# Kernel tuning notes

Hardware: AMD Instinct MI355X
Metric: run time of the kernel (lower is better)

The kernel has to match this reference:

```python
import jax, jax.numpy as jnp
import numpy as np

N_HEADS = 16
ROPE_BASE = 10000.0


def setup_inputs() -> dict:
    key = jax.random.key(0)
    k1, k2, k3 = jax.random.split(key, 3)
    B, L, D = 2, 2048, 2048
    x = jax.random.normal(k1, (B, L, D), dtype=jnp.float32)
    w_qkv = jax.random.normal(k2, (D, 3 * D), dtype=jnp.float32) * (1.0 / np.sqrt(D))
    w_out = jax.random.normal(k3, (D, D), dtype=jnp.float32) * (1.0 / np.sqrt(D))
    return {"x": x, "w_qkv": w_qkv, "w_out": w_out}


def _rope_cos_sin(L, head_dim, dtype):
    # inv_freq over even dims, freqs duplicated across both halves (HF convention)
    inv_freq = 1.0 / (ROPE_BASE ** (jnp.arange(0, head_dim, 2, dtype=jnp.float32) / head_dim))
    freqs = jnp.arange(L, dtype=jnp.float32)[:, None] * inv_freq[None, :]  # [L, hd/2]
    emb = jnp.concatenate([freqs, freqs], axis=-1)  # [L, hd]
    return jnp.cos(emb).astype(dtype), jnp.sin(emb).astype(dtype)


def _rotate_half(t):
    h = t.shape[-1] // 2
    return jnp.concatenate([-t[..., h:], t[..., :h]], axis=-1)


def reference(x, w_qkv, w_out):
    B, L, D = x.shape
    H = N_HEADS
    hd = D // H
    qkv = x @ w_qkv  # [B, L, 3D]
    q, k, v = jnp.split(qkv, 3, axis=-1)

    def heads(t):  # [B, L, D] -> [B, H, L, hd]
        return t.reshape(B, L, H, hd).transpose(0, 2, 1, 3)

    q, k, v = heads(q), heads(k), heads(v)
    cos, sin = _rope_cos_sin(L, hd, x.dtype)  # [L, hd] broadcast over B,H
    q = q * cos + _rotate_half(q) * sin
    k = k * cos + _rotate_half(k) * sin
    # SDPA, no mask, no dropout (eval), not causal
    scale = 1.0 / np.sqrt(hd)
    scores = jnp.einsum('bhld,bhsd->bhls', q, k) * scale
    attn = jax.nn.softmax(scores, axis=-1)
    y = jnp.einsum('bhls,bhsd->bhld', attn, v)  # [B, H, L, hd]
    y = y.transpose(0, 2, 1, 3).reshape(B, L, D)
    return y @ w_out
```

## Files before the change

kernel.cpp:

```cpp
#include <hip/hip_runtime.h>

typedef __attribute__((ext_vector_type(8))) short bf16x8;
typedef __attribute__((ext_vector_type(8))) unsigned short u16x8;
typedef __attribute__((ext_vector_type(4))) float f32x4;
typedef __attribute__((ext_vector_type(16))) float f32x16;
typedef __attribute__((ext_vector_type(4))) unsigned short u16x4;
typedef __attribute__((ext_vector_type(4))) unsigned int u32x4;
typedef unsigned int u32;

#define BB 2
#define LL 2048
#define DD 2048
#define HH 16
#define HDIM 128
#define MM 4096
#define NQKV 6144

__device__ __forceinline__ unsigned short f2bf(float f) {
    unsigned int u = __builtin_bit_cast(unsigned int, f);
    u += 0x7FFFu + ((u >> 16) & 1u);
    return (unsigned short)(u >> 16);
}
__device__ __forceinline__ float bf2f(unsigned short h) {
    unsigned int u = ((unsigned int)h) << 16;
    return __builtin_bit_cast(float, u);
}

__device__ __forceinline__ void gload16(const unsigned short* g, unsigned short* l) {
    __builtin_amdgcn_global_load_lds((const __attribute__((address_space(1))) void*)g,
                                     (__attribute__((address_space(3))) void*)l, 16, 0, 0);
}

__device__ __forceinline__ u32 cvtpk(float lo, float hi) {
    u32 r;
    asm("v_cvt_pk_bf16_f32 %0, %1, %2" : "=v"(r) : "v"(lo), "v"(hi));
    return r;
}
__device__ __forceinline__ void plswap(u32& a, u32& b) {
    asm("v_permlane32_swap_b32 %0, %1" : "+v"(a), "+v"(b));
}

__global__ __launch_bounds__(256) void k_cvt_bf16(const float* __restrict__ in,
                                                  unsigned short* __restrict__ out,
                                                  int n4) {
    int i = blockIdx.x * 256 + threadIdx.x;
    if (i < n4) {
        float4 v = reinterpret_cast<const float4*>(in)[i];
        u16x4 o;
        o[0] = f2bf(v.x); o[1] = f2bf(v.y); o[2] = f2bf(v.z); o[3] = f2bf(v.w);
        reinterpret_cast<u16x4*>(out)[i] = o;
    }
}

__global__ __launch_bounds__(256) void k_cvt_T(const float* __restrict__ in,
                                               unsigned short* __restrict__ out,
                                               int K, int N) {
    __shared__ unsigned short t[64][72];
    int n0 = blockIdx.x * 64, k0 = blockIdx.y * 64;
    int tid = threadIdx.x;
    int tr = tid >> 4, tc = tid & 15;
    #pragma unroll
    for (int i = 0; i < 4; ++i) {
        int k = i * 16 + tr;
        float4 v = *reinterpret_cast<const float4*>(in + (size_t)(k0 + k) * N + n0 + tc * 4);
        t[tc * 4 + 0][k] = f2bf(v.x);
        t[tc * 4 + 1][k] = f2bf(v.y);
        t[tc * 4 + 2][k] = f2bf(v.z);
        t[tc * 4 + 3][k] = f2bf(v.w);
    }
    __syncthreads();
    #pragma unroll
    for (int i = 0; i < 4; ++i) {
        int n = i * 16 + tr;
        u16x4 o = *reinterpret_cast<u16x4*>(&t[n][tc * 4]);
        *reinterpret_cast<u16x4*>(out + (size_t)(n0 + n) * K + k0 + tc * 4) = o;
    }
}

__global__ __launch_bounds__(256) void k_transV(const unsigned short* __restrict__ in,
                                                unsigned short* __restrict__ out) {
    __shared__ unsigned short t[64][68];
    int l0 = blockIdx.x * 64, d0 = blockIdx.y * 64;
    int bh = blockIdx.z;
    const unsigned short* ib = in + (size_t)bh * LL * HDIM;
    unsigned short* ob = out + (size_t)bh * HDIM * LL;
    int tid = threadIdx.x;
    int tr = tid >> 4, tc = tid & 15;
    #pragma unroll
    for (int i = 0; i < 4; ++i) {
        int l = i * 16 + tr;
        u16x4 v = *reinterpret_cast<const u16x4*>(ib + (size_t)(l0 + l) * HDIM + d0 + tc * 4);
        t[tc * 4 + 0][l] = v[0];
        t[tc * 4 + 1][l] = v[1];
        t[tc * 4 + 2][l] = v[2];
        t[tc * 4 + 3][l] = v[3];
    }
    __syncthreads();
    #pragma unroll
    for (int i = 0; i < 4; ++i) {
        int d = i * 16 + tr;
        u16x4 o = *reinterpret_cast<u16x4*>(&t[d][tc * 4]);
        *reinterpret_cast<u16x4*>(ob + (size_t)(d0 + d) * LL + l0 + tc * 4) = o;
    }
}

__global__ __launch_bounds__(256) void k_rope_table(float* __restrict__ ct,
                                                    float* __restrict__ st) {
    int idx = blockIdx.x * 256 + threadIdx.x;
    if (idx >= LL * 64) return;
    int pos = idx >> 6, d = idx & 63;
    float freq = __expf(-(float)d * (9.210340371976184f / 64.0f));
    float ang = (float)pos * freq;
    ct[idx] = cosf(ang);
    st[idx] = sinf(ang);
}

__global__ __launch_bounds__(256) void k_rope_apply(unsigned short* __restrict__ Q,
                                                    unsigned short* __restrict__ K,
                                                    const float* __restrict__ ct,
                                                    const float* __restrict__ st) {
    int idx = blockIdx.x * 256 + threadIdx.x;
    int d = idx & 63;
    int pos = (idx >> 6) & (LL - 1);
    int bh = idx >> 17;
    size_t base = ((size_t)bh * LL + pos) * HDIM;
    float c = ct[pos * 64 + d], s = st[pos * 64 + d];
    float q0 = bf2f(Q[base + d]), q1 = bf2f(Q[base + d + 64]);
    Q[base + d]      = f2bf(q0 * c - q1 * s);
    Q[base + d + 64] = f2bf(q1 * c + q0 * s);
    float k0 = bf2f(K[base + d]), k1 = bf2f(K[base + d + 64]);
    K[base + d]      = f2bf(k0 * c - k1 * s);
    K[base + d + 64] = f2bf(k1 * c + k0 * s);
}

__global__ __launch_bounds__(512, 2) void k_gemm384(const unsigned short* __restrict__ A,
                                                    const unsigned short* __restrict__ Bt,
                                                    unsigned short* __restrict__ outQ,
                                                    unsigned short* __restrict__ outK,
                                                    unsigned short* __restrict__ outV) {
    __shared__ unsigned short sm[3 * 20480];
    const int Kn = DD;
    const int tid = threadIdx.x;
    const int lane = tid & 63, w = tid >> 6;
    const int wm = w >> 2, wn = w & 3;
    const int lrow = lane & 15, lgrp = lane >> 4;
    const int NT = Kn / 32;

    int orig = blockIdx.x;
    int tau = (orig & 7) * 32 + (orig >> 3);
    const int m0 = (tau & 15) * 256, n0 = (tau >> 4) * 384;

    const int srow = lane >> 2, scol = lane & 3;
    const int scolg = ((scol ^ ((srow >> 1) & 3)) * 8);
    const int fcol  = ((lgrp ^ ((lrow >> 1) & 3)) * 8);

    f32x4 acc[8][6] = {};

    auto stageA = [&](int t, int r) {
        unsigned short* dst = sm + (t % 3) * 20480 + (r * 128 + w * 16) * 32;
        gload16(A + (size_t)(m0 + r * 128 + w * 16 + srow) * Kn + t * 32 + scolg, dst);
    };
    auto stageB = [&](int t, int r) {
        unsigned short* dst = sm + (t % 3) * 20480 + 8192 + (r * 128 + w * 16) * 32;
        gload16(Bt + (size_t)(n0 + r * 128 + w * 16 + srow) * Kn + t * 32 + scolg, dst);
    };

    auto body = [&](int t, bool doStage) {
        unsigned short* bufA = sm + (t % 3) * 20480;
        unsigned short* bufB = bufA + 8192;
        bf16x8 af[8], bfr[2];
        #pragma unroll
        for (int f = 0; f < 8; ++f)
            af[f] = *reinterpret_cast<const bf16x8*>(bufA + (wm * 128 + f * 16 + lrow) * 32 + fcol);
        bfr[0] = *reinterpret_cast<const bf16x8*>(bufB + (wn * 96 + 0 * 16 + lrow) * 32 + fcol);
        bfr[1] = *reinterpret_cast<const bf16x8*>(bufB + (wn * 96 + 1 * 16 + lrow) * 32 + fcol);
        if (doStage) { stageA(t + 2, 0); stageA(t + 2, 1); }
        __builtin_amdgcn_s_barrier();
        __builtin_amdgcn_s_setprio(1);
        #pragma unroll
        for (int fm = 0; fm < 8; ++fm)
            #pragma unroll
            for (int j = 0; j < 2; ++j)
                acc[fm][j] = __builtin_amdgcn_mfma_f32_16x16x32_bf16(af[fm], bfr[j], acc[fm][j], 0, 0, 0);
        __builtin_amdgcn_s_setprio(0);
        bfr[0] = *reinterpret_cast<const bf16x8*>(bufB + (wn * 96 + 2 * 16 + lrow) * 32 + fcol);
        bfr[1] = *reinterpret_cast<const bf16x8*>(bufB + (wn * 96 + 3 * 16 + lrow) * 32 + fcol);
        if (doStage) { stageB(t + 2, 0); stageB(t + 2, 1); }
        __builtin_amdgcn_s_barrier();
        __builtin_amdgcn_s_setprio(1);
        #pragma unroll
        for (int fm = 0; fm < 8; ++fm)
            #pragma unroll
            for (int j = 0; j < 2; ++j)
                acc[fm][2 + j] = __builtin_amdgcn_mfma_f32_16x16x32_bf16(af[fm], bfr[j], acc[fm][2 + j], 0, 0, 0);
        __builtin_amdgcn_s_setprio(0);
        bfr[0] = *reinterpret_cast<const bf16x8*>(bufB + (wn * 96 + 4 * 16 + lrow) * 32 + fcol);
        bfr[1] = *reinterpret_cast<const bf16x8*>(bufB + (wn * 96 + 5 * 16 + lrow) * 32 + fcol);
        if (doStage) { stageB(t + 2, 2); }
        __builtin_amdgcn_s_barrier();
        __builtin_amdgcn_s_setprio(1);
        #pragma unroll
        for (int fm = 0; fm < 8; ++fm)
            #pragma unroll
            for (int j = 0; j < 2; ++j)
                acc[fm][4 + j] = __builtin_amdgcn_mfma_f32_16x16x32_bf16(af[fm], bfr[j], acc[fm][4 + j], 0, 0, 0);
        __builtin_amdgcn_s_setprio(0);
    };

    stageA(0, 0); stageA(0, 1); stageB(0, 0); stageB(0, 1); stageB(0, 2);
    stageA(1, 0); stageA(1, 1); stageB(1, 0); stageB(1, 1); stageB(1, 2);
    asm volatile("s_waitcnt vmcnt(5)" ::: "memory");
    __builtin_amdgcn_s_barrier();

    for (int t = 0; t < NT - 2; ++t) {
        body(t, true);
        asm volatile("s_waitcnt vmcnt(5)" ::: "memory");
        __builtin_amdgcn_s_barrier();
    }
    body(NT - 2, false);
    asm volatile("s_waitcnt vmcnt(0)" ::: "memory");
    __builtin_amdgcn_s_barrier();
    body(NT - 1, false);

    #pragma unroll
    for (int fm = 0; fm < 8; ++fm) {
        int mrow = m0 + wm * 128 + fm * 16 + lgrp * 4;
        #pragma unroll
        for (int fn = 0; fn < 6; ++fn) {
            int ncol = n0 + wn * 96 + fn * 16 + lrow;
            int which = ncol >> 11;
            int rr = ncol & (DD - 1);
            int h = rr >> 7, d = rr & (HDIM - 1);
            unsigned short* dst = (which == 0) ? outQ : ((which == 1) ? outK : outV);
            #pragma unroll
            for (int i = 0; i < 4; ++i) {
                int m = mrow + i;
                int b = m >> 11, pos = m & (LL - 1);
                dst[((size_t)(b * HH + h) * LL + pos) * HDIM + d] = f2bf(acc[fm][fn][i]);
            }
        }
    }
}

__global__ __launch_bounds__(512) void k_gemm2x(const unsigned short* __restrict__ A,
                                                const unsigned short* __restrict__ Bt,
                                                float* __restrict__ outC) {
    __shared__ unsigned short sm[4 * 12288];
    const int Kn = DD, Nn = DD;
    const int tid = threadIdx.x;
    const int lane = tid & 63, w = tid >> 6;
    const int wm = w >> 1, wn = w & 1;
    const int lrow = lane & 15, lgrp = lane >> 4;
    const int NT = Kn / 32;

    int orig = blockIdx.x;
    int tau = (orig & 7) * 32 + (orig >> 3);
    const int m0 = (tau & 15) * 256, n0 = (tau >> 4) * 128;

    const int srow = lane >> 2, scol = lane & 3;
    const int scolg = ((scol ^ ((srow >> 1) & 3)) * 8);
    const int fcol  = ((lgrp ^ ((lrow >> 1) & 3)) * 8);

    f32x4 acc[4][4] = {};

    auto stage = [&](int t) {
        const int kb = t * 32;
        unsigned short* buf = sm + (t & 3) * 12288;
        gload16(A  + (size_t)(m0 + w * 16 + srow) * Kn + kb + scolg,        buf + w * 512);
        gload16(A  + (size_t)(m0 + 128 + w * 16 + srow) * Kn + kb + scolg,  buf + 4096 + w * 512);
        gload16(Bt + (size_t)(n0 + w * 16 + srow) * Kn + kb + scolg,        buf + 8192 + w * 512);
    };

    auto tile_body = [&](int t, bool do_stage) {
        unsigned short* buf = sm + (t & 3) * 12288;
        bf16x8 af[4], bfr[4];
        #pragma unroll
        for (int f = 0; f < 4; ++f)
            af[f] = *reinterpret_cast<const bf16x8*>(buf + (wm * 64 + f * 16 + lrow) * 32 + fcol);
        #pragma unroll
        for (int f = 0; f < 4; ++f)
            bfr[f] = *reinterpret_cast<const bf16x8*>(buf + 8192 + (wn * 64 + f * 16 + lrow) * 32 + fcol);
        if (do_stage) stage(t + 3);
        __builtin_amdgcn_s_barrier();
        __builtin_amdgcn_s_setprio(1);
        #pragma unroll
        for (int fm = 0; fm < 4; ++fm)
            #pragma unroll
            for (int fn = 0; fn < 4; ++fn)
                acc[fm][fn] = __builtin_amdgcn_mfma_f32_16x16x32_bf16(af[fm], bfr[fn], acc[fm][fn], 0, 0, 0);
        __builtin_amdgcn_s_setprio(0);
    };

    stage(0); stage(1); stage(2);
    asm volatile("s_waitcnt vmcnt(6)" ::: "memory");
    __builtin_amdgcn_s_barrier();

    for (int t = 0; t < NT - 3; ++t) {
        tile_body(t, true);
        asm volatile("s_waitcnt vmcnt(6)" ::: "memory");
        __builtin_amdgcn_s_barrier();
    }
    tile_body(NT - 3, false);
    asm volatile("s_waitcnt vmcnt(3)" ::: "memory");
    __builtin_amdgcn_s_barrier();
    tile_body(NT - 2, false);
    asm volatile("s_waitcnt vmcnt(0)" ::: "memory");
    __builtin_amdgcn_s_barrier();
    tile_body(NT - 1, false);

    #pragma unroll
    for (int fm = 0; fm < 4; ++fm) {
        int mrow = m0 + wm * 64 + fm * 16 + lgrp * 4;
        #pragma unroll
        for (int fn = 0; fn < 4; ++fn) {
            int ncol = n0 + wn * 64 + fn * 16 + lrow;
            #pragma unroll
            for (int i = 0; i < 4; ++i)
                outC[(size_t)(mrow + i) * (size_t)Nn + ncol] = acc[fm][fn][i];
        }
    }
}

__global__ __launch_bounds__(256, 2) void k_attn(const unsigned short* __restrict__ Q,
                                                 const unsigned short* __restrict__ K,
                                                 const unsigned short* __restrict__ Vt,
                                                 unsigned short* __restrict__ Y) {
    __shared__ unsigned short Kl[2][64][136];
    __shared__ unsigned short VTl[2][128][72];
    int tid = threadIdx.x;
    int lane = tid & 63, w = tid >> 6;
    int l31 = lane & 31, hl = lane >> 5;
    int orig = blockIdx.x;
    int id = (orig & 7) * 64 + (orig >> 3);
    int bh = id >> 4, qt = id & 15;
    int b = bh >> 4, hh = bh & 15;
    const unsigned short* Qb = Q  + (size_t)bh * LL * HDIM;
    const unsigned short* Kb = K  + (size_t)bh * LL * HDIM;
    const unsigned short* Vb = Vt + (size_t)bh * HDIM * LL;
    int q0 = qt * 128 + w * 32;

    bf16x8 qf[8];
    #pragma unroll
    for (int kk = 0; kk < 8; ++kk)
        qf[kk] = *reinterpret_cast<const bf16x8*>(
            Qb + (size_t)(q0 + l31) * HDIM + kk * 16 + hl * 8);

    f32x16 accO[4] = {};
    f32x16 accL = {};
    bf16x8 ones;
    #pragma unroll
    for (int j = 0; j < 8; ++j) ones[j] = (short)0x3F80;
    const float scale = 0.08838834764831845f;

    u16x8 kr[4], vr[4];
    auto sload = [&](int kt) {
        #pragma unroll
        for (int i = 0; i < 4; ++i) {
            int c = i * 256 + tid;
            kr[i] = *reinterpret_cast<const u16x8*>(Kb + (size_t)(kt * 64 + (c >> 4)) * HDIM + (c & 15) * 8);
            vr[i] = *reinterpret_cast<const u16x8*>(Vb + (size_t)(c >> 3) * LL + kt * 64 + (c & 7) * 8);
        }
    };
    auto swrite = [&](int buf) {
        #pragma unroll
        for (int i = 0; i < 4; ++i) {
            int c = i * 256 + tid;
            *reinterpret_cast<u16x8*>(&Kl[buf][c >> 4][(c & 15) * 8]) = kr[i];
            *reinterpret_cast<u16x8*>(&VTl[buf][c >> 3][(c & 7) * 8]) = vr[i];
        }
    };

    sload(0);
    swrite(0);
    __syncthreads();

    for (int kt = 0; kt < LL / 64; ++kt) {
        int cb = kt & 1;
        if (kt + 1 < LL / 64) sload(kt + 1);

        f32x16 s[2] = {};
        __builtin_amdgcn_s_setprio(1);
        #pragma unroll
        for (int kk = 0; kk < 8; ++kk) {
            bf16x8 kf0 = *reinterpret_cast<const bf16x8*>(&Kl[cb][l31][kk * 16 + hl * 8]);
            bf16x8 kf1 = *reinterpret_cast<const bf16x8*>(&Kl[cb][32 + l31][kk * 16 + hl * 8]);
            s[0] = __builtin_amdgcn_mfma_f32_32x32x16_bf16(kf0, qf[kk], s[0], 0, 0, 0);
            s[1] = __builtin_amdgcn_mfma_f32_32x32x16_bf16(kf1, qf[kk], s[1], 0, 0, 0);
        }
        __builtin_amdgcn_s_setprio(0);

        bf16x8 pa[2][2];
        #pragma unroll
        for (int kn = 0; kn < 2; ++kn) {
            float p[16];
            #pragma unroll
            for (int r = 0; r < 16; ++r) p[r] = __expf(s[kn][r] * scale);
            #pragma unroll
            for (int ksub = 0; ksub < 2; ++ksub) {
                const int bse = ksub * 8;
                u32 a0 = cvtpk(p[bse + 0], p[bse + 1]);
                u32 a1 = cvtpk(p[bse + 2], p[bse + 3]);
                u32 b0 = cvtpk(p[bse + 4], p[bse + 5]);
                u32 b1 = cvtpk(p[bse + 6], p[bse + 7]);
                plswap(a0, b0);
                plswap(a1, b1);
                u32x4 fw; fw[0] = a0; fw[1] = a1; fw[2] = b0; fw[3] = b1;
                pa[kn][ksub] = __builtin_bit_cast(bf16x8, fw);
            }
        }

        __builtin_amdgcn_s_setprio(1);
        #pragma unroll
        for (int kn = 0; kn < 2; ++kn)
            #pragma unroll
            for (int ksub = 0; ksub < 2; ++ksub) {
                accL = __builtin_amdgcn_mfma_f32_32x32x16_bf16(pa[kn][ksub], ones, accL, 0, 0, 0);
                #pragma unroll
                for (int dn = 0; dn < 4; ++dn) {
                    bf16x8 vf = *reinterpret_cast<const bf16x8*>(
                        &VTl[cb][dn * 32 + l31][kn * 32 + ksub * 16 + hl * 8]);
                    accO[dn] = __builtin_amdgcn_mfma_f32_32x32x16_bf16(pa[kn][ksub], vf, accO[dn], 0, 0, 0);
                }
            }
        __builtin_amdgcn_s_setprio(0);

        if (kt + 1 < LL / 64) swrite(cb ^ 1);
        __syncthreads();
    }

    #pragma unroll
    for (int r = 0; r < 16; ++r) {
        float inv = 1.0f / accL[r];
        int qrow = (r & 3) + 8 * (r >> 2) + 4 * hl;
        int pos = q0 + qrow;
        #pragma unroll
        for (int dn = 0; dn < 4; ++dn) {
            int d = dn * 32 + l31;
            Y[((size_t)b * LL + pos) * DD + hh * HDIM + d] = f2bf(accO[dn][r] * inv);
        }
    }
}

extern "C" void kernel_launch(void* const* d_in, const int* in_sizes, int n_in,
                              void* d_out, int out_size, void* d_ws, size_t ws_size,
                              hipStream_t stream) {
    const float* x     = (const float*)d_in[0];
    const float* wqkv  = (const float*)d_in[1];
    const float* wout  = (const float*)d_in[2];
    float* out = (float*)d_out;

    char* ws = (char*)d_ws;
    size_t off = 0;
    auto take = [&](size_t bytes) { char* p = ws + off; off += (bytes + 255) & ~(size_t)255; return p; };
    unsigned short* xb    = (unsigned short*)take((size_t)MM * DD * 2);
    unsigned short* wqkvT = (unsigned short*)take((size_t)DD * NQKV * 2);
    unsigned short* woutT = (unsigned short*)take((size_t)DD * DD * 2);
    unsigned short* Qb    = (unsigned short*)take((size_t)BB * HH * LL * HDIM * 2);
    unsigned short* Kb    = (unsigned short*)take((size_t)BB * HH * LL * HDIM * 2);
    unsigned short* Vb    = (unsigned short*)take((size_t)BB * HH * LL * HDIM * 2);
    unsigned short* Yb    = (unsigned short*)take((size_t)MM * DD * 2);
    float* ct             = (float*)take((size_t)LL * 64 * 4);
    float* st             = (float*)take((size_t)LL * 64 * 4);
    if (off > ws_size) return;
    unsigned short* VtB = xb;

    k_cvt_bf16<<<(MM * DD / 4 + 255) / 256, 256, 0, stream>>>(x, xb, MM * DD / 4);
    k_cvt_T<<<dim3(NQKV / 64, DD / 64), 256, 0, stream>>>(wqkv, wqkvT, DD, NQKV);
    k_cvt_T<<<dim3(DD / 64, DD / 64), 256, 0, stream>>>(wout, woutT, DD, DD);
    k_rope_table<<<(LL * 64 + 255) / 256, 256, 0, stream>>>(ct, st);

    k_gemm384<<<256, 512, 0, stream>>>(xb, wqkvT, Qb, Kb, Vb);
    k_transV<<<dim3(LL / 64, HDIM / 64, BB * HH), 256, 0, stream>>>(Vb, VtB);
    k_rope_apply<<<(BB * HH * LL * 64) / 256, 256, 0, stream>>>(Qb, Kb, ct, st);
    k_attn<<<BB * HH * (LL / 128), 256, 0, stream>>>(Qb, Kb, VtB, Yb);
    k_gemm2x<<<256, 512, 0, stream>>>(Yb, woutT, out);
}
```

Measured before the change: 254.2 us.

## Fuse V transpose into QKV GEMM epilogue and reorder MFMA phases

The QKV GEMM epilogue now writes V directly in transposed [bh][d][pos] layout with 4-wide vector stores, which removes the separate k_transV kernel launch and its extra read and write of V. V gets its own workspace buffer instead of aliasing xb. The GEMM inner body is also regrouped: A fragments are loaded in two halves and B fragments in two groups of three, so each barrier phase issues 12 or 24 MFMAs in a different interleave. This can change register pressure and how well LDS reads overlap with compute.

```diff
diff --git a/kernel.cpp b/kernel.cpp
--- a/kernel.cpp
+++ b/kernel.cpp
@@ -74,33 +74,6 @@
         int n = i * 16 + tr;
         u16x4 o = *reinterpret_cast<u16x4*>(&t[n][tc * 4]);
         *reinterpret_cast<u16x4*>(out + (size_t)(n0 + n) * K + k0 + tc * 4) = o;
-    }
-}
-
-__global__ __launch_bounds__(256) void k_transV(const unsigned short* __restrict__ in,
-                                                unsigned short* __restrict__ out) {
-    __shared__ unsigned short t[64][68];
-    int l0 = blockIdx.x * 64, d0 = blockIdx.y * 64;
-    int bh = blockIdx.z;
-    const unsigned short* ib = in + (size_t)bh * LL * HDIM;
-    unsigned short* ob = out + (size_t)bh * HDIM * LL;
-    int tid = threadIdx.x;
-    int tr = tid >> 4, tc = tid & 15;
-    #pragma unroll
-    for (int i = 0; i < 4; ++i) {
-        int l = i * 16 + tr;
-        u16x4 v = *reinterpret_cast<const u16x4*>(ib + (size_t)(l0 + l) * HDIM + d0 + tc * 4);
-        t[tc * 4 + 0][l] = v[0];
-        t[tc * 4 + 1][l] = v[1];
-        t[tc * 4 + 2][l] = v[2];
-        t[tc * 4 + 3][l] = v[3];
-    }
-    __syncthreads();
-    #pragma unroll
-    for (int i = 0; i < 4; ++i) {
-        int d = i * 16 + tr;
-        u16x4 o = *reinterpret_cast<u16x4*>(&t[d][tc * 4]);
-        *reinterpret_cast<u16x4*>(ob + (size_t)(d0 + d) * LL + l0 + tc * 4) = o;
     }
 }
 
@@ -137,7 +110,7 @@
                                                     const unsigned short* __restrict__ Bt,
                                                     unsigned short* __restrict__ outQ,
                                                     unsigned short* __restrict__ outK,
-                                                    unsigned short* __restrict__ outV) {
+                                                    unsigned short* __restrict__ outVt) {
     __shared__ unsigned short sm[3 * 20480];
     const int Kn = DD;
     const int tid = threadIdx.x;
@@ -168,42 +141,45 @@
     auto body = [&](int t, bool doStage) {
         unsigned short* bufA = sm + (t % 3) * 20480;
         unsigned short* bufB = bufA + 8192;
-        bf16x8 af[8], bfr[2];
-        #pragma unroll
-        for (int f = 0; f < 8; ++f)
+        bf16x8 af[8], bfr[6];
+        #pragma unroll
+        for (int f = 0; f < 4; ++f)
             af[f] = *reinterpret_cast<const bf16x8*>(bufA + (wm * 128 + f * 16 + lrow) * 32 + fcol);
-        bfr[0] = *reinterpret_cast<const bf16x8*>(bufB + (wn * 96 + 0 * 16 + lrow) * 32 + fcol);
-        bfr[1] = *reinterpret_cast<const bf16x8*>(bufB + (wn * 96 + 1 * 16 + lrow) * 32 + fcol);
+        #pragma unroll
+        for (int j = 0; j < 3; ++j)
+            bfr[j] = *reinterpret_cast<const bf16x8*>(bufB + (wn * 96 + j * 16 + lrow) * 32 + fcol);
         if (doStage) { stageA(t + 2, 0); stageA(t + 2, 1); }
         __builtin_amdgcn_s_barrier();
         __builtin_amdgcn_s_setprio(1);
         #pragma unroll
+        for (int fm = 0; fm < 4; ++fm)
+            #pragma unroll
+            for (int fn = 0; fn < 3; ++fn)
+                acc[fm][fn] = __builtin_amdgcn_mfma_f32_16x16x32_bf16(af[fm], bfr[fn], acc[fm][fn], 0, 0, 0);
+        __builtin_amdgcn_s_setprio(0);
+        #pragma unroll
+        for (int f = 4; f < 8; ++f)
+            af[f] = *reinterpret_cast<const bf16x8*>(bufA + (wm * 128 + f * 16 + lrow) * 32 + fcol);
+        if (doStage) { stageB(t + 2, 0); stageB(t + 2, 1); }
+        __builtin_amdgcn_s_barrier();
+        __builtin_amdgcn_s_setprio(1);
+        #pragma unroll
+        for (int fm = 4; fm < 8; ++fm)
+            #pragma unroll
+            for (int fn = 0; fn < 3; ++fn)
+                acc[fm][fn] = __builtin_amdgcn_mfma_f32_16x16x32_bf16(af[fm], bfr[fn], acc[fm][fn], 0, 0, 0);
+        __builtin_amdgcn_s_setprio(0);
+        #pragma unroll
+        for (int j = 3; j < 6; ++j)
+            bfr[j] = *reinterpret_cast<const bf16x8*>(bufB + (wn * 96 + j * 16 + lrow) * 32 + fcol);
+        if (doStage) { stageB(t + 2, 2); }
+        __builtin_amdgcn_s_barrier();
+        __builtin_amdgcn_s_setprio(1);
+        #pragma unroll
         for (int fm = 0; fm < 8; ++fm)
             #pragma unroll
-            for (int j = 0; j < 2; ++j)
-                acc[fm][j] = __builtin_amdgcn_mfma_f32_16x16x32_bf16(af[fm], bfr[j], acc[fm][j], 0, 0, 0);
-        __builtin_amdgcn_s_setprio(0);
-        bfr[0] = *reinterpret_cast<const bf16x8*>(bufB + (wn * 96 + 2 * 16 + lrow) * 32 + fcol);
-        bfr[1] = *reinterpret_cast<const bf16x8*>(bufB + (wn * 96 + 3 * 16 + lrow) * 32 + fcol);
-        if (doStage) { stageB(t + 2, 0); stageB(t + 2, 1); }
-        __builtin_amdgcn_s_barrier();
-        __builtin_amdgcn_s_setprio(1);
-        #pragma unroll
-        for (int fm = 0; fm < 8; ++fm)
-            #pragma unroll
-            for (int j = 0; j < 2; ++j)
-                acc[fm][2 + j] = __builtin_amdgcn_mfma_f32_16x16x32_bf16(af[fm], bfr[j], acc[fm][2 + j], 0, 0, 0);
-        __builtin_amdgcn_s_setprio(0);
-        bfr[0] = *reinterpret_cast<const bf16x8*>(bufB + (wn * 96 + 4 * 16 + lrow) * 32 + fcol);
-        bfr[1] = *reinterpret_cast<const bf16x8*>(bufB + (wn * 96 + 5 * 16 + lrow) * 32 + fcol);
-        if (doStage) { stageB(t + 2, 2); }
-        __builtin_amdgcn_s_barrier();
-        __builtin_amdgcn_s_setprio(1);
-        #pragma unroll
-        for (int fm = 0; fm < 8; ++fm)
-            #pragma unroll
-            for (int j = 0; j < 2; ++j)
-                acc[fm][4 + j] = __builtin_amdgcn_mfma_f32_16x16x32_bf16(af[fm], bfr[j], acc[fm][4 + j], 0, 0, 0);
+            for (int fn = 3; fn < 6; ++fn)
+                acc[fm][fn] = __builtin_amdgcn_mfma_f32_16x16x32_bf16(af[fm], bfr[fn], acc[fm][fn], 0, 0, 0);
         __builtin_amdgcn_s_setprio(0);
     };
 
@@ -225,18 +201,23 @@
     #pragma unroll
     for (int fm = 0; fm < 8; ++fm) {
         int mrow = m0 + wm * 128 + fm * 16 + lgrp * 4;
+        int b = mrow >> 11, pos = mrow & (LL - 1);
         #pragma unroll
         for (int fn = 0; fn < 6; ++fn) {
             int ncol = n0 + wn * 96 + fn * 16 + lrow;
             int which = ncol >> 11;
             int rr = ncol & (DD - 1);
             int h = rr >> 7, d = rr & (HDIM - 1);
-            unsigned short* dst = (which == 0) ? outQ : ((which == 1) ? outK : outV);
-            #pragma unroll
-            for (int i = 0; i < 4; ++i) {
-                int m = mrow + i;
-                int b = m >> 11, pos = m & (LL - 1);
-                dst[((size_t)(b * HH + h) * LL + pos) * HDIM + d] = f2bf(acc[fm][fn][i]);
+            if (which == 2) {
+                u16x4 o;
+                #pragma unroll
+                for (int i = 0; i < 4; ++i) o[i] = f2bf(acc[fm][fn][i]);
+                *reinterpret_cast<u16x4*>(outVt + ((size_t)(b * HH + h) * HDIM + d) * LL + pos) = o;
+            } else {
+                unsigned short* dst = which ? outK : outQ;
+                #pragma unroll
+                for (int i = 0; i < 4; ++i)
+                    dst[((size_t)(b * HH + h) * LL + pos + i) * HDIM + d] = f2bf(acc[fm][fn][i]);
             }
         }
     }
@@ -457,20 +438,18 @@
     unsigned short* woutT = (unsigned short*)take((size_t)DD * DD * 2);
     unsigned short* Qb    = (unsigned short*)take((size_t)BB * HH * LL * HDIM * 2);
     unsigned short* Kb    = (unsigned short*)take((size_t)BB * HH * LL * HDIM * 2);
-    unsigned short* Vb    = (unsigned short*)take((size_t)BB * HH * LL * HDIM * 2);
+    unsigned short* VtB   = (unsigned short*)take((size_t)BB * HH * LL * HDIM * 2);
     unsigned short* Yb    = (unsigned short*)take((size_t)MM * DD * 2);
     float* ct             = (float*)take((size_t)LL * 64 * 4);
     float* st             = (float*)take((size_t)LL * 64 * 4);
     if (off > ws_size) return;
-    unsigned short* VtB = xb;
 
     k_cvt_bf16<<<(MM * DD / 4 + 255) / 256, 256, 0, stream>>>(x, xb, MM * DD / 4);
     k_cvt_T<<<dim3(NQKV / 64, DD / 64), 256, 0, stream>>>(wqkv, wqkvT, DD, NQKV);
     k_cvt_T<<<dim3(DD / 64, DD / 64), 256, 0, stream>>>(wout, woutT, DD, DD);
     k_rope_table<<<(LL * 64 + 255) / 256, 256, 0, stream>>>(ct, st);
 
-    k_gemm384<<<256, 512, 0, stream>>>(xb, wqkvT, Qb, Kb, Vb);
-    k_transV<<<dim3(LL / 64, HDIM / 64, BB * HH), 256, 0, stream>>>(Vb, VtB);
+    k_gemm384<<<256, 512, 0, stream>>>(xb, wqkvT, Qb, Kb, VtB);
     k_rope_apply<<<(BB * HH * LL * 64) / 256, 256, 0, stream>>>(Qb, Kb, ct, st);
     k_attn<<<BB * HH * (LL / 128), 256, 0, stream>>>(Qb, Kb, VtB, Yb);
     k_gemm2x<<<256, 512, 0, stream>>>(Yb, woutT, out);
```

Result: slower. 264.1 us (+3.9%).
